# Kernel optimization log

Hardware: AMD Instinct MI355X
Metric: run time of the kernel (lower is better)

Reference implementation:

```python
import jax, jax.numpy as jnp
import numpy as np

ENC, STR_H, CELL_H, ATTN = 512, 256, 512, 512
B, L = 64, 1024


def setup_inputs() -> dict:
    key = jax.random.key(0)
    ks = jax.random.split(key, 12)
    s = lambda fan_in: 1.0 / np.sqrt(fan_in)
    return {
        "encoded_features_map": jax.random.normal(ks[0], (B, L, ENC), jnp.float32),
        "structural_hidden_state": jax.random.normal(ks[1], (1, B, STR_H), jnp.float32),
        "cell_content_hidden_state": jax.random.normal(ks[2], (1, B, CELL_H), jnp.float32),
        "W_enc": jax.random.uniform(ks[3], (ENC, ATTN), jnp.float32, -s(ENC), s(ENC)),
        "b_enc": jax.random.uniform(ks[4], (ATTN,), jnp.float32, -s(ENC), s(ENC)),
        "W_str": jax.random.uniform(ks[5], (STR_H, ATTN), jnp.float32, -s(STR_H), s(STR_H)),
        "b_str": jax.random.uniform(ks[6], (ATTN,), jnp.float32, -s(STR_H), s(STR_H)),
        "W_cell": jax.random.uniform(ks[7], (CELL_H, ATTN), jnp.float32, -s(CELL_H), s(CELL_H)),
        "b_cell": jax.random.uniform(ks[8], (ATTN,), jnp.float32, -s(CELL_H), s(CELL_H)),
        "W_comb": jax.random.uniform(ks[9], (ATTN, 1), jnp.float32, -s(ATTN), s(ATTN)),
        "b_comb": jax.random.uniform(ks[10], (1,), jnp.float32, -s(ATTN), s(ATTN)),
    }


def reference(encoded_features_map, structural_hidden_state, cell_content_hidden_state,
              W_enc, b_enc, W_str, b_str, W_cell, b_cell, W_comb, b_comb):
    # [B, L, A] projection of encoder features
    a_enc = jnp.einsum("ble,ea->bla", encoded_features_map, W_enc) + b_enc
    # [B, A] projections of the two hidden states (squeeze layer dim)
    a_str = structural_hidden_state[0] @ W_str + b_str
    a_cell = cell_content_hidden_state[0] @ W_cell + b_cell
    # broadcast add + ReLU + scalar score: [B, L]
    h = jax.nn.relu(a_enc + a_str[:, None, :] + a_cell[:, None, :])
    scores = jnp.einsum("bla,ao->bl", h, W_comb) + b_comb[0]
    weights = jax.nn.softmax(scores, axis=1)  # over sequence dim
    # weighted sum over L -> [B, ENC]
    context = jnp.einsum("bl,ble->be", weights, encoded_features_map)
    return context
```

## Files before the change

### kernel.cpp

```cpp
#include <hip/hip_runtime.h>
#include <stdint.h>

#define ENC_D 512
#define ATTN_D 512
#define STR_D 256
#define CELL_D 512
#define BATCH 64
#define SEQ 1024
#define NROWS (BATCH * SEQ)

typedef __bf16 bf16x8 __attribute__((ext_vector_type(8)));
typedef float f32x4 __attribute__((ext_vector_type(4)));

__device__ __forceinline__ unsigned short f2bf(float f) {
    unsigned int u = __float_as_uint(f);
    u += 0x7fffu + ((u >> 16) & 1u);
    return (unsigned short)(u >> 16);
}

__device__ __forceinline__ bf16x8 cvt8(const float4 a, const float4 b) {
    bf16x8 r;
    r[0] = (__bf16)a.x; r[1] = (__bf16)a.y; r[2] = (__bf16)a.z; r[3] = (__bf16)a.w;
    r[4] = (__bf16)b.x; r[5] = (__bf16)b.y; r[6] = (__bf16)b.z; r[7] = (__bf16)b.w;
    return r;
}

__device__ __forceinline__ void lds_cp16(void* l, const void* g) {
    __builtin_amdgcn_global_load_lds(
        (const __attribute__((address_space(1))) unsigned int*)g,
        (__attribute__((address_space(3))) unsigned int*)l, 16, 0, 0);
}

#define BAR_VM4() asm volatile("s_waitcnt vmcnt(4)\n\ts_barrier" ::: "memory")
#define BAR_VM0() asm volatile("s_waitcnt vmcnt(0)\n\ts_barrier" ::: "memory")

__global__ __launch_bounds__(256) void k_prep(const float* __restrict__ W,
                                              unsigned short* __restrict__ WF,
                                              const float* __restrict__ str,
                                              const float* __restrict__ cell,
                                              const float* __restrict__ Wstr,
                                              const float* __restrict__ Wcell,
                                              float* __restrict__ bpart) {
    __shared__ char smraw[64 * 68 * 2];
    const int bx = blockIdx.x, t = threadIdx.x;

    if (bx < 64) {
        unsigned short* T = (unsigned short*)smraw;
        const int ei = bx >> 3, ni = bx & 7;
        const int e0 = ei * 64, n0 = ni * 64;
#pragma unroll
        for (int i = 0; i < 4; ++i) {
            const int idx = t + i * 256;
            const int r = idx >> 4, c4 = idx & 15;
            const float4 v = *(const float4*)(W + (size_t)(e0 + r) * ATTN_D + n0 + c4 * 4);
            T[(c4 * 4 + 0) * 68 + r] = f2bf(v.x);
            T[(c4 * 4 + 1) * 68 + r] = f2bf(v.y);
            T[(c4 * 4 + 2) * 68 + r] = f2bf(v.z);
            T[(c4 * 4 + 3) * 68 + r] = f2bf(v.w);
        }
        __syncthreads();
#pragma unroll
        for (int i = 0; i < 2; ++i) {
            const int q = t + i * 256;
            const int n = q >> 3, ge = q & 7;
            union { unsigned short s[8]; uint4 u; } o;
#pragma unroll
            for (int j = 0; j < 8; ++j) o.s[j] = T[n * 68 + ge * 8 + j];
            const int ng = n0 + n;
            const int g = ei * 8 + ge;
            const int nt = ng >> 4, c = ng & 15;
            const int ks = g >> 2, quad = g & 3;
            const int gi = nt * 1024 + ks * 64 + quad * 16 + c;
            *(uint4*)(WF + (size_t)gi * 8) = o.u;
        }
    } else {
        float* sj = (float*)smraw;
        float* red = (float*)smraw + 64;
        const int q = bx - 64;
        const int b = q / 12, jq = q - b * 12;
        const float* hvec;
        const float* Wbase;
        if (jq < 4) { hvec = str + b * STR_D + jq * 64;         Wbase = Wstr + (size_t)(jq * 64) * ATTN_D; }
        else        { hvec = cell + b * CELL_D + (jq - 4) * 64; Wbase = Wcell + (size_t)((jq - 4) * 64) * ATTN_D; }
        if (t < 64) sj[t] = hvec[t];
        __syncthreads();
        const int h = t >> 7, a4 = t & 127;
        f32x4 acc = {0.f, 0.f, 0.f, 0.f};
#pragma unroll 8
        for (int i = h * 32; i < h * 32 + 32; ++i) {
            const float s = sj[i];
            const float4 wv = *(const float4*)(Wbase + (size_t)i * ATTN_D + a4 * 4);
            acc[0] += s * wv.x; acc[1] += s * wv.y; acc[2] += s * wv.z; acc[3] += s * wv.w;
        }
        if (h == 1) *(f32x4*)(red + a4 * 4) = acc;
        __syncthreads();
        if (h == 0) {
            const f32x4 o = *(const f32x4*)(red + a4 * 4);
            acc[0] += o[0]; acc[1] += o[1]; acc[2] += o[2]; acc[3] += o[3];
            *(f32x4*)(bpart + (size_t)(jq * BATCH + b) * ATTN_D + a4 * 4) = acc;
        }
    }
}

__global__ __launch_bounds__(512, 1) void k_scores(const float* __restrict__ E,
                                                   const unsigned short* __restrict__ WF,
                                                   const float* __restrict__ bpart,
                                                   const float* __restrict__ b_enc,
                                                   const float* __restrict__ b_str,
                                                   const float* __restrict__ b_cell,
                                                   const float* __restrict__ Wcomb,
                                                   float* __restrict__ ctxp,
                                                   float* __restrict__ stats) {
    __shared__ unsigned short buf[3][16384];
    __shared__ float sbias[512];
    __shared__ float sWc[512];
    __shared__ float sx[256];
    __shared__ float ex[256];
    __shared__ float red[3][512];
    __shared__ float rtmp[8];

    const int tid = threadIdx.x;
    const int r0 = blockIdx.x * 256;
    const int b = blockIdx.x >> 2;
    const int w = tid >> 6, lane = tid & 63;
    const int quad = lane >> 4, c = lane & 15;

#pragma unroll
    for (int p = 0; p < 2; ++p)
#pragma unroll
        for (int i = 0; i < 4; ++i)
            lds_cp16((char*)&buf[p][0] + i * 8192 + tid * 16,
                     (const char*)WF + (size_t)p * 32768 + i * 8192 + tid * 16);

    if (tid < 128) {
        const int a = tid * 4;
        const float4 be = *(const float4*)(b_enc + a);
        const float4 bs = *(const float4*)(b_str + a);
        const float4 bc = *(const float4*)(b_cell + a);
        f32x4 s;
        s[0] = be.x + bs.x + bc.x; s[1] = be.y + bs.y + bc.y;
        s[2] = be.z + bs.z + bc.z; s[3] = be.w + bs.w + bc.w;
#pragma unroll
        for (int jq = 0; jq < 12; ++jq) {
            const float4 p = *(const float4*)(bpart + (size_t)(jq * BATCH + b) * ATTN_D + a);
            s[0] += p.x; s[1] += p.y; s[2] += p.z; s[3] += p.w;
        }
        *(f32x4*)(sbias + a) = s;
        const float4 wcv = *(const float4*)(Wcomb + a);
        f32x4 wc4; wc4[0] = wcv.x; wc4[1] = wcv.y; wc4[2] = wcv.z; wc4[3] = wcv.w;
        *(f32x4*)(sWc + a) = wc4;
    }

    bf16x8 afr[2][16];
#pragma unroll
    for (int m = 0; m < 2; ++m) {
        const float* Ep = E + (size_t)(r0 + w * 32 + m * 16 + c) * ENC_D + quad * 8;
#pragma unroll
        for (int ks = 0; ks < 16; ++ks) {
            const float4 v0 = *(const float4*)(Ep + ks * 32);
            const float4 v1 = *(const float4*)(Ep + ks * 32 + 4);
            afr[m][ks] = cvt8(v0, v1);
        }
    }

    float sc0[4] = {0.f, 0.f, 0.f, 0.f};
    float sc1[4] = {0.f, 0.f, 0.f, 0.f};

    __syncthreads();

    int cbuf = 0, sbuf = 2;
    for (int ch = 0; ch < 16; ++ch) {
        if (ch < 14) {
            const char* gsrc = (const char*)WF + (size_t)(ch + 2) * 32768;
            char* ldst = (char*)&buf[sbuf][0];
#pragma unroll
            for (int i = 0; i < 4; ++i)
                lds_cp16(ldst + i * 8192 + tid * 16, gsrc + i * 8192 + tid * 16);
        }

        const unsigned short* wb = &buf[cbuf][0];
        f32x4 a0e = {0.f,0.f,0.f,0.f}, a0o = {0.f,0.f,0.f,0.f};
        f32x4 a1e = {0.f,0.f,0.f,0.f}, a1o = {0.f,0.f,0.f,0.f};
        f32x4 b0e = {0.f,0.f,0.f,0.f}, b0o = {0.f,0.f,0.f,0.f};
        f32x4 b1e = {0.f,0.f,0.f,0.f}, b1o = {0.f,0.f,0.f,0.f};
#pragma unroll
        for (int ks = 0; ks < 16; ks += 4) {
            const bf16x8 f0 = *(const bf16x8*)(wb + ((ks + 0) * 64 + lane) * 8);
            const bf16x8 f1 = *(const bf16x8*)(wb + ((ks + 1) * 64 + lane) * 8);
            const bf16x8 f2 = *(const bf16x8*)(wb + ((ks + 2) * 64 + lane) * 8);
            const bf16x8 f3 = *(const bf16x8*)(wb + ((ks + 3) * 64 + lane) * 8);
            const bf16x8 g0 = *(const bf16x8*)(wb + 8192 + ((ks + 0) * 64 + lane) * 8);
            const bf16x8 g1 = *(const bf16x8*)(wb + 8192 + ((ks + 1) * 64 + lane) * 8);
            const bf16x8 g2 = *(const bf16x8*)(wb + 8192 + ((ks + 2) * 64 + lane) * 8);
            const bf16x8 g3 = *(const bf16x8*)(wb + 8192 + ((ks + 3) * 64 + lane) * 8);
            a0e = __builtin_amdgcn_mfma_f32_16x16x32_bf16(afr[0][ks + 0], f0, a0e, 0, 0, 0);
            a1e = __builtin_amdgcn_mfma_f32_16x16x32_bf16(afr[1][ks + 0], f0, a1e, 0, 0, 0);
            a0o = __builtin_amdgcn_mfma_f32_16x16x32_bf16(afr[0][ks + 1], f1, a0o, 0, 0, 0);
            a1o = __builtin_amdgcn_mfma_f32_16x16x32_bf16(afr[1][ks + 1], f1, a1o, 0, 0, 0);
            b0e = __builtin_amdgcn_mfma_f32_16x16x32_bf16(afr[0][ks + 0], g0, b0e, 0, 0, 0);
            b1e = __builtin_amdgcn_mfma_f32_16x16x32_bf16(afr[1][ks + 0], g0, b1e, 0, 0, 0);
            b0o = __builtin_amdgcn_mfma_f32_16x16x32_bf16(afr[0][ks + 1], g1, b0o, 0, 0, 0);
            b1o = __builtin_amdgcn_mfma_f32_16x16x32_bf16(afr[1][ks + 1], g1, b1o, 0, 0, 0);
            a0e = __builtin_amdgcn_mfma_f32_16x16x32_bf16(afr[0][ks + 2], f2, a0e, 0, 0, 0);
            a1e = __builtin_amdgcn_mfma_f32_16x16x32_bf16(afr[1][ks + 2], f2, a1e, 0, 0, 0);
            a0o = __builtin_amdgcn_mfma_f32_16x16x32_bf16(afr[0][ks + 3], f3, a0o, 0, 0, 0);
            a1o = __builtin_amdgcn_mfma_f32_16x16x32_bf16(afr[1][ks + 3], f3, a1o, 0, 0, 0);
            b0e = __builtin_amdgcn_mfma_f32_16x16x32_bf16(afr[0][ks + 2], g2, b0e, 0, 0, 0);
            b1e = __builtin_amdgcn_mfma_f32_16x16x32_bf16(afr[1][ks + 2], g2, b1e, 0, 0, 0);
            b0o = __builtin_amdgcn_mfma_f32_16x16x32_bf16(afr[0][ks + 3], g3, b0o, 0, 0, 0);
            b1o = __builtin_amdgcn_mfma_f32_16x16x32_bf16(afr[1][ks + 3], g3, b1o, 0, 0, 0);
        }

        const int n0 = ch * 32 + c;
        const float bi0 = sbias[n0], wc0 = sWc[n0];
        const float bi1 = sbias[n0 + 16], wc1 = sWc[n0 + 16];
#pragma unroll
        for (int r = 0; r < 4; ++r) {
            float v;
            v = (a0e[r] + a0o[r]) + bi0; sc0[r] += (v > 0.f ? v : 0.f) * wc0;
            v = (b0e[r] + b0o[r]) + bi1; sc0[r] += (v > 0.f ? v : 0.f) * wc1;
            v = (a1e[r] + a1o[r]) + bi0; sc1[r] += (v > 0.f ? v : 0.f) * wc0;
            v = (b1e[r] + b1o[r]) + bi1; sc1[r] += (v > 0.f ? v : 0.f) * wc1;
        }

        cbuf = (cbuf == 2) ? 0 : cbuf + 1;
        sbuf = (sbuf == 2) ? 0 : sbuf + 1;
        if (ch < 15) {
            if (ch < 14) BAR_VM4();
            else         BAR_VM0();
        }
    }

#pragma unroll
    for (int r = 0; r < 4; ++r) {
        float v0 = sc0[r], v1 = sc1[r];
        v0 += __shfl_xor(v0, 1); v1 += __shfl_xor(v1, 1);
        v0 += __shfl_xor(v0, 2); v1 += __shfl_xor(v1, 2);
        v0 += __shfl_xor(v0, 4); v1 += __shfl_xor(v1, 4);
        sc0[r] = v0 + __shfl_xor(v0, 8);
        sc1[r] = v1 + __shfl_xor(v1, 8);
    }
    if (c == 0) {
        const int l0 = w * 32 + quad * 4;
#pragma unroll
        for (int r = 0; r < 4; ++r) sx[l0 + r] = sc0[r];
#pragma unroll
        for (int r = 0; r < 4; ++r) sx[l0 + 16 + r] = sc1[r];
    }
    __syncthreads();

    if (tid < 256) {
        float v = sx[tid];
        float mm = v;
#pragma unroll
        for (int o = 32; o > 0; o >>= 1) mm = fmaxf(mm, __shfl_xor(mm, o));
        if (lane == 0) rtmp[w] = mm;
    }
    __syncthreads();
    const float m_p = fmaxf(fmaxf(rtmp[0], rtmp[1]), fmaxf(rtmp[2], rtmp[3]));
    if (tid < 256) {
        const float e = __expf(sx[tid] - m_p);
        ex[tid] = e;
        float ss = e;
#pragma unroll
        for (int o = 32; o > 0; o >>= 1) ss += __shfl_xor(ss, o);
        if (lane == 0) rtmp[4 + w] = ss;
    }
    __syncthreads();
    if (tid == 0) {
        stats[blockIdx.x * 2 + 0] = m_p;
        stats[blockIdx.x * 2 + 1] = rtmp[4] + rtmp[5] + rtmp[6] + rtmp[7];
    }

    {
        const int g = tid >> 7, col4 = tid & 127;
        const float* Ep = E + (size_t)(r0 + g * 64) * ENC_D + col4 * 4;
        f32x4 accA = {0.f, 0.f, 0.f, 0.f};
        f32x4 accB = {0.f, 0.f, 0.f, 0.f};
#pragma unroll 8
        for (int l = 0; l < 64; l += 2) {
            const float4 eA = *(const float4*)(Ep + (size_t)l * ENC_D);
            const float4 eB = *(const float4*)(Ep + (size_t)(l + 1) * ENC_D);
            const float wA = ex[g * 64 + l];
            const float wB = ex[g * 64 + l + 1];
            accA[0] += wA * eA.x; accA[1] += wA * eA.y;
            accA[2] += wA * eA.z; accA[3] += wA * eA.w;
            accB[0] += wB * eB.x; accB[1] += wB * eB.y;
            accB[2] += wB * eB.z; accB[3] += wB * eB.w;
        }
        f32x4 acc;
        acc[0] = accA[0] + accB[0]; acc[1] = accA[1] + accB[1];
        acc[2] = accA[2] + accB[2]; acc[3] = accA[3] + accB[3];
        if (g > 0) *(f32x4*)(&red[g - 1][col4 * 4]) = acc;
        __syncthreads();
        if (g == 0) {
            const f32x4 r1 = *(const f32x4*)(&red[0][col4 * 4]);
            const f32x4 r2 = *(const f32x4*)(&red[1][col4 * 4]);
            const f32x4 r3 = *(const f32x4*)(&red[2][col4 * 4]);
            acc[0] += r1[0] + r2[0] + r3[0];
            acc[1] += r1[1] + r2[1] + r3[1];
            acc[2] += r1[2] + r2[2] + r3[2];
            acc[3] += r1[3] + r2[3] + r3[3];
            *(f32x4*)(ctxp + (size_t)blockIdx.x * 512 + col4 * 4) = acc;
        }
    }
}

__global__ __launch_bounds__(128) void k_final(const float* __restrict__ ctxp,
                                               const float* __restrict__ stats,
                                               float* __restrict__ out) {
    const int b = blockIdx.x, t = threadIdx.x;
    const float m0 = stats[(b * 4 + 0) * 2], z0 = stats[(b * 4 + 0) * 2 + 1];
    const float m1 = stats[(b * 4 + 1) * 2], z1 = stats[(b * 4 + 1) * 2 + 1];
    const float m2 = stats[(b * 4 + 2) * 2], z2 = stats[(b * 4 + 2) * 2 + 1];
    const float m3 = stats[(b * 4 + 3) * 2], z3 = stats[(b * 4 + 3) * 2 + 1];
    const float m = fmaxf(fmaxf(m0, m1), fmaxf(m2, m3));
    const float a0 = __expf(m0 - m), a1 = __expf(m1 - m);
    const float a2 = __expf(m2 - m), a3 = __expf(m3 - m);
    const float invD = 1.f / (z0 * a0 + z1 * a1 + z2 * a2 + z3 * a3);

    const float4 c0 = *(const float4*)(ctxp + (size_t)(b * 4 + 0) * 512 + t * 4);
    const float4 c1 = *(const float4*)(ctxp + (size_t)(b * 4 + 1) * 512 + t * 4);
    const float4 c2 = *(const float4*)(ctxp + (size_t)(b * 4 + 2) * 512 + t * 4);
    const float4 c3 = *(const float4*)(ctxp + (size_t)(b * 4 + 3) * 512 + t * 4);
    f32x4 o;
    o[0] = (c0.x * a0 + c1.x * a1 + c2.x * a2 + c3.x * a3) * invD;
    o[1] = (c0.y * a0 + c1.y * a1 + c2.y * a2 + c3.y * a3) * invD;
    o[2] = (c0.z * a0 + c1.z * a1 + c2.z * a2 + c3.z * a3) * invD;
    o[3] = (c0.w * a0 + c1.w * a1 + c2.w * a2 + c3.w * a3) * invD;
    *(f32x4*)(out + (size_t)b * ENC_D + t * 4) = o;
}

extern "C" void kernel_launch(void* const* d_in, const int* in_sizes, int n_in,
                              void* d_out, int out_size, void* d_ws, size_t ws_size,
                              hipStream_t stream) {
    const float* E      = (const float*)d_in[0];
    const float* str    = (const float*)d_in[1];
    const float* cell   = (const float*)d_in[2];
    const float* Wenc   = (const float*)d_in[3];
    const float* b_enc  = (const float*)d_in[4];
    const float* Wstr   = (const float*)d_in[5];
    const float* b_str  = (const float*)d_in[6];
    const float* Wcell  = (const float*)d_in[7];
    const float* b_cell = (const float*)d_in[8];
    const float* Wcomb  = (const float*)d_in[9];
    float* out = (float*)d_out;

    char* ws = (char*)d_ws;
    unsigned short* WF = (unsigned short*)ws;
    float* bpart = (float*)(ws + (512 << 10));
    float* ctxp  = (float*)(ws + (512 << 10) + (1536 << 10));
    float* stats = (float*)(ws + (512 << 10) + (2048 << 10));

    k_prep<<<832, 256, 0, stream>>>(Wenc, WF, str, cell, Wstr, Wcell, bpart);
    k_scores<<<NROWS / 256, 512, 0, stream>>>(E, WF, bpart, b_enc, b_str, b_cell, Wcomb, ctxp, stats);
    k_final<<<BATCH, 128, 0, stream>>>(ctxp, stats, out);
}
```

Baseline: 262.8 us.

## Stage encoder A-fragments through LDS with pipelined async global-to-LDS copies

The A operand (encoder rows) was loaded with direct per-lane float4 global loads and converted to bf16 in registers. It is now streamed into a per-wave LDS staging area with async global_load_lds copies, double-buffered in 8 pieces with vmcnt waits, then read back from LDS and converted. The shared memory is merged into one raw region so this staging can reuse the space later taken by the weight triple buffer. The aim is more outstanding memory traffic and better-coalesced global reads. The cost is extra LDS round trips, an added barrier, and a larger shared footprint.

Measured after the change: 270.0 us. 1.03x slower.

```diff
diff --git a/kernel.cpp b/kernel.cpp
--- a/kernel.cpp
+++ b/kernel.cpp
@@ -33,6 +33,8 @@
 
 #define BAR_VM4() asm volatile("s_waitcnt vmcnt(4)\n\ts_barrier" ::: "memory")
 #define BAR_VM0() asm volatile("s_waitcnt vmcnt(0)\n\ts_barrier" ::: "memory")
+#define WAIT_VM8() asm volatile("s_waitcnt vmcnt(8)" ::: "memory")
+#define WAIT_VM0() asm volatile("s_waitcnt vmcnt(0)" ::: "memory")
 
 __global__ __launch_bounds__(256) void k_prep(const float* __restrict__ W,
                                               unsigned short* __restrict__ WF,
@@ -111,25 +113,68 @@
                                                    const float* __restrict__ Wcomb,
                                                    float* __restrict__ ctxp,
                                                    float* __restrict__ stats) {
-    __shared__ unsigned short buf[3][16384];
-    __shared__ float sbias[512];
-    __shared__ float sWc[512];
-    __shared__ float sx[256];
-    __shared__ float ex[256];
-    __shared__ float red[3][512];
-    __shared__ float rtmp[8];
+    __shared__ char smem[131072 + 12352];
+    float* sbias = (float*)(smem + 131072);
+    float* sWc   = (float*)(smem + 131072 + 2048);
+    float* sx    = (float*)(smem + 131072 + 4096);
+    float* ex    = (float*)(smem + 131072 + 5120);
+    float* redp  = (float*)(smem + 131072 + 6144);
+    float* rtmp  = (float*)(smem + 131072 + 12288);
 
     const int tid = threadIdx.x;
     const int r0 = blockIdx.x * 256;
     const int b = blockIdx.x >> 2;
     const int w = tid >> 6, lane = tid & 63;
     const int quad = lane >> 4, c = lane & 15;
+    const int rl0 = lane & 15;
+    const int cqv = lane >> 4;
+
+    bf16x8 afr[2][16];
+    {
+        char* Ab = smem + w * 16384;
+        const float* Esrc = E + (size_t)(r0 + w * 32) * ENC_D;
+
+#define ISSUE_PIECE(sp)                                                        \
+        do {                                                                   \
+            char* dst_ = Ab + (((sp) & 1) ? 8192 : 0);                         \
+            _Pragma("unroll")                                                  \
+            for (int i = 0; i < 8; ++i) {                                      \
+                const int row_ = rl0 + ((i & 1) << 4);                         \
+                const int colq_ = (sp) * 16 + cqv + ((i >> 1) << 2);           \
+                lds_cp16(dst_ + i * 1024 + lane * 16,                          \
+                         Esrc + (size_t)row_ * ENC_D + colq_ * 4);             \
+            }                                                                  \
+        } while (0)
+
+        ISSUE_PIECE(0);
+        ISSUE_PIECE(1);
+#pragma unroll
+        for (int s = 0; s < 8; ++s) {
+            if (s < 7) WAIT_VM8();
+            else       WAIT_VM0();
+            const char* Pb = Ab + ((s & 1) ? 8192 : 0);
+#pragma unroll
+            for (int m = 0; m < 2; ++m)
+#pragma unroll
+                for (int d = 0; d < 2; ++d) {
+                    const int x0 = d * 8 + quad * 2;
+                    const int x1 = x0 + 1;
+                    const float4 g0 = *(const float4*)(Pb + (m + 2 * (x0 >> 2)) * 1024 + (c + 16 * (x0 & 3)) * 16);
+                    const float4 g1 = *(const float4*)(Pb + (m + 2 * (x1 >> 2)) * 1024 + (c + 16 * (x1 & 3)) * 16);
+                    afr[m][2 * s + d] = cvt8(g0, g1);
+                }
+            if (s < 6) ISSUE_PIECE(s + 2);
+        }
+#undef ISSUE_PIECE
+    }
+
+    __syncthreads();
 
 #pragma unroll
     for (int p = 0; p < 2; ++p)
 #pragma unroll
         for (int i = 0; i < 4; ++i)
-            lds_cp16((char*)&buf[p][0] + i * 8192 + tid * 16,
+            lds_cp16(smem + p * 32768 + i * 8192 + tid * 16,
                      (const char*)WF + (size_t)p * 32768 + i * 8192 + tid * 16);
 
     if (tid < 128) {
@@ -151,18 +196,6 @@
         *(f32x4*)(sWc + a) = wc4;
     }
 
-    bf16x8 afr[2][16];
-#pragma unroll
-    for (int m = 0; m < 2; ++m) {
-        const float* Ep = E + (size_t)(r0 + w * 32 + m * 16 + c) * ENC_D + quad * 8;
-#pragma unroll
-        for (int ks = 0; ks < 16; ++ks) {
-            const float4 v0 = *(const float4*)(Ep + ks * 32);
-            const float4 v1 = *(const float4*)(Ep + ks * 32 + 4);
-            afr[m][ks] = cvt8(v0, v1);
-        }
-    }
-
     float sc0[4] = {0.f, 0.f, 0.f, 0.f};
     float sc1[4] = {0.f, 0.f, 0.f, 0.f};
 
@@ -172,13 +205,13 @@
     for (int ch = 0; ch < 16; ++ch) {
         if (ch < 14) {
             const char* gsrc = (const char*)WF + (size_t)(ch + 2) * 32768;
-            char* ldst = (char*)&buf[sbuf][0];
+            char* ldst = smem + sbuf * 32768;
 #pragma unroll
             for (int i = 0; i < 4; ++i)
                 lds_cp16(ldst + i * 8192 + tid * 16, gsrc + i * 8192 + tid * 16);
         }
 
-        const unsigned short* wb = &buf[cbuf][0];
+        const unsigned short* wb = (const unsigned short*)(smem + cbuf * 32768);
         f32x4 a0e = {0.f,0.f,0.f,0.f}, a0o = {0.f,0.f,0.f,0.f};
         f32x4 a1e = {0.f,0.f,0.f,0.f}, a1o = {0.f,0.f,0.f,0.f};
         f32x4 b0e = {0.f,0.f,0.f,0.f}, b0o = {0.f,0.f,0.f,0.f};
@@ -189,10 +222,10 @@
             const bf16x8 f1 = *(const bf16x8*)(wb + ((ks + 1) * 64 + lane) * 8);
             const bf16x8 f2 = *(const bf16x8*)(wb + ((ks + 2) * 64 + lane) * 8);
             const bf16x8 f3 = *(const bf16x8*)(wb + ((ks + 3) * 64 + lane) * 8);
-            const bf16x8 g0 = *(const bf16x8*)(wb + 8192 + ((ks + 0) * 64 + lane) * 8);
-            const bf16x8 g1 = *(const bf16x8*)(wb + 8192 + ((ks + 1) * 64 + lane) * 8);
-            const bf16x8 g2 = *(const bf16x8*)(wb + 8192 + ((ks + 2) * 64 + lane) * 8);
-            const bf16x8 g3 = *(const bf16x8*)(wb + 8192 + ((ks + 3) * 64 + lane) * 8);
+            const bf16x8 g0 = *(const bf16x8*)(wb + 4096 * 2 + ((ks + 0) * 64 + lane) * 8);
+            const bf16x8 g1 = *(const bf16x8*)(wb + 4096 * 2 + ((ks + 1) * 64 + lane) * 8);
+            const bf16x8 g2 = *(const bf16x8*)(wb + 4096 * 2 + ((ks + 2) * 64 + lane) * 8);
+            const bf16x8 g3 = *(const bf16x8*)(wb + 4096 * 2 + ((ks + 3) * 64 + lane) * 8);
             a0e = __builtin_amdgcn_mfma_f32_16x16x32_bf16(afr[0][ks + 0], f0, a0e, 0, 0, 0);
             a1e = __builtin_amdgcn_mfma_f32_16x16x32_bf16(afr[1][ks + 0], f0, a1e, 0, 0, 0);
             a0o = __builtin_amdgcn_mfma_f32_16x16x32_bf16(afr[0][ks + 1], f1, a0o, 0, 0, 0);
@@ -291,12 +324,12 @@
         f32x4 acc;
         acc[0] = accA[0] + accB[0]; acc[1] = accA[1] + accB[1];
         acc[2] = accA[2] + accB[2]; acc[3] = accA[3] + accB[3];
-        if (g > 0) *(f32x4*)(&red[g - 1][col4 * 4]) = acc;
+        if (g > 0) *(f32x4*)(redp + (g - 1) * 512 + col4 * 4) = acc;
         __syncthreads();
         if (g == 0) {
-            const f32x4 r1 = *(const f32x4*)(&red[0][col4 * 4]);
-            const f32x4 r2 = *(const f32x4*)(&red[1][col4 * 4]);
-            const f32x4 r3 = *(const f32x4*)(&red[2][col4 * 4]);
+            const f32x4 r1 = *(const f32x4*)(redp + 0 * 512 + col4 * 4);
+            const f32x4 r2 = *(const f32x4*)(redp + 1 * 512 + col4 * 4);
+            const f32x4 r3 = *(const f32x4*)(redp + 2 * 512 + col4 * 4);
             acc[0] += r1[0] + r2[0] + r3[0];
             acc[1] += r1[1] + r2[1] + r3[1];
             acc[2] += r1[2] + r2[2] + r3[2];
```

## Fuse final softmax-merge into scores kernel via last-block atomic counter

Applied to the files above, without the earlier changes.

Removes the separate k_final launch. Each scores block increments a per-batch atomic counter, and the last of the four blocks for a batch merges the partial max/sum stats and context into the output. The counter is reset by an extra block in k_prep. The diff also batches all the encoder-feature loads before the bf16 conversions, split by a sched_barrier, so more memory requests are in flight at once. This adds threadfence and atomic cost per block and a serial tail in the last block.

Result: slower. 323.7 us (+23.2%).

```diff
diff --git a/kernel.cpp b/kernel.cpp
--- a/kernel.cpp
+++ b/kernel.cpp
@@ -40,7 +40,8 @@
                                               const float* __restrict__ cell,
                                               const float* __restrict__ Wstr,
                                               const float* __restrict__ Wcell,
-                                              float* __restrict__ bpart) {
+                                              float* __restrict__ bpart,
+                                              unsigned int* __restrict__ cnt) {
     __shared__ char smraw[64 * 68 * 2];
     const int bx = blockIdx.x, t = threadIdx.x;
 
@@ -73,7 +74,7 @@
             const int gi = nt * 1024 + ks * 64 + quad * 16 + c;
             *(uint4*)(WF + (size_t)gi * 8) = o.u;
         }
-    } else {
+    } else if (bx < 832) {
         float* sj = (float*)smraw;
         float* red = (float*)smraw + 64;
         const int q = bx - 64;
@@ -99,6 +100,8 @@
             acc[0] += o[0]; acc[1] += o[1]; acc[2] += o[2]; acc[3] += o[3];
             *(f32x4*)(bpart + (size_t)(jq * BATCH + b) * ATTN_D + a4 * 4) = acc;
         }
+    } else {
+        if (t < BATCH) cnt[t] = 0u;
     }
 }
 
@@ -110,7 +113,9 @@
                                                    const float* __restrict__ b_cell,
                                                    const float* __restrict__ Wcomb,
                                                    float* __restrict__ ctxp,
-                                                   float* __restrict__ stats) {
+                                                   float* __restrict__ stats,
+                                                   unsigned int* __restrict__ cnt,
+                                                   float* __restrict__ out) {
     __shared__ unsigned short buf[3][16384];
     __shared__ float sbias[512];
     __shared__ float sWc[512];
@@ -118,6 +123,7 @@
     __shared__ float ex[256];
     __shared__ float red[3][512];
     __shared__ float rtmp[8];
+    __shared__ int lastf;
 
     const int tid = threadIdx.x;
     const int r0 = blockIdx.x * 256;
@@ -155,12 +161,16 @@
 #pragma unroll
     for (int m = 0; m < 2; ++m) {
         const float* Ep = E + (size_t)(r0 + w * 32 + m * 16 + c) * ENC_D + quad * 8;
+        float4 t0[16], t1[16];
 #pragma unroll
         for (int ks = 0; ks < 16; ++ks) {
-            const float4 v0 = *(const float4*)(Ep + ks * 32);
-            const float4 v1 = *(const float4*)(Ep + ks * 32 + 4);
-            afr[m][ks] = cvt8(v0, v1);
-        }
+            t0[ks] = *(const float4*)(Ep + ks * 32);
+            t1[ks] = *(const float4*)(Ep + ks * 32 + 4);
+        }
+        __builtin_amdgcn_sched_barrier(0);
+#pragma unroll
+        for (int ks = 0; ks < 16; ++ks)
+            afr[m][ks] = cvt8(t0[ks], t1[ks]);
     }
 
     float sc0[4] = {0.f, 0.f, 0.f, 0.f};
@@ -304,31 +314,30 @@
             *(f32x4*)(ctxp + (size_t)blockIdx.x * 512 + col4 * 4) = acc;
         }
     }
-}
-
-__global__ __launch_bounds__(128) void k_final(const float* __restrict__ ctxp,
-                                               const float* __restrict__ stats,
-                                               float* __restrict__ out) {
-    const int b = blockIdx.x, t = threadIdx.x;
-    const float m0 = stats[(b * 4 + 0) * 2], z0 = stats[(b * 4 + 0) * 2 + 1];
-    const float m1 = stats[(b * 4 + 1) * 2], z1 = stats[(b * 4 + 1) * 2 + 1];
-    const float m2 = stats[(b * 4 + 2) * 2], z2 = stats[(b * 4 + 2) * 2 + 1];
-    const float m3 = stats[(b * 4 + 3) * 2], z3 = stats[(b * 4 + 3) * 2 + 1];
-    const float m = fmaxf(fmaxf(m0, m1), fmaxf(m2, m3));
-    const float a0 = __expf(m0 - m), a1 = __expf(m1 - m);
-    const float a2 = __expf(m2 - m), a3 = __expf(m3 - m);
-    const float invD = 1.f / (z0 * a0 + z1 * a1 + z2 * a2 + z3 * a3);
-
-    const float4 c0 = *(const float4*)(ctxp + (size_t)(b * 4 + 0) * 512 + t * 4);
-    const float4 c1 = *(const float4*)(ctxp + (size_t)(b * 4 + 1) * 512 + t * 4);
-    const float4 c2 = *(const float4*)(ctxp + (size_t)(b * 4 + 2) * 512 + t * 4);
-    const float4 c3 = *(const float4*)(ctxp + (size_t)(b * 4 + 3) * 512 + t * 4);
-    f32x4 o;
-    o[0] = (c0.x * a0 + c1.x * a1 + c2.x * a2 + c3.x * a3) * invD;
-    o[1] = (c0.y * a0 + c1.y * a1 + c2.y * a2 + c3.y * a3) * invD;
-    o[2] = (c0.z * a0 + c1.z * a1 + c2.z * a2 + c3.z * a3) * invD;
-    o[3] = (c0.w * a0 + c1.w * a1 + c2.w * a2 + c3.w * a3) * invD;
-    *(f32x4*)(out + (size_t)b * ENC_D + t * 4) = o;
+
+    __threadfence();
+    __syncthreads();
+    if (tid == 0) lastf = (atomicAdd(&cnt[b], 1u) == 3u) ? 1 : 0;
+    __syncthreads();
+    if (lastf) {
+        __threadfence();
+        float mp[4], zp[4];
+#pragma unroll
+        for (int p = 0; p < 4; ++p) {
+            mp[p] = stats[(b * 4 + p) * 2];
+            zp[p] = stats[(b * 4 + p) * 2 + 1];
+        }
+        const float m = fmaxf(fmaxf(mp[0], mp[1]), fmaxf(mp[2], mp[3]));
+        float a[4], D = 0.f;
+#pragma unroll
+        for (int p = 0; p < 4; ++p) { a[p] = __expf(mp[p] - m); D += zp[p] * a[p]; }
+        const float invD = 1.f / D;
+        float o = 0.f;
+#pragma unroll
+        for (int p = 0; p < 4; ++p)
+            o += ctxp[(size_t)(b * 4 + p) * 512 + tid] * a[p];
+        out[(size_t)b * ENC_D + tid] = o * invD;
+    }
 }
 
 extern "C" void kernel_launch(void* const* d_in, const int* in_sizes, int n_in,
@@ -351,8 +360,9 @@
     float* bpart = (float*)(ws + (512 << 10));
     float* ctxp  = (float*)(ws + (512 << 10) + (1536 << 10));
     float* stats = (float*)(ws + (512 << 10) + (2048 << 10));
-
-    k_prep<<<832, 256, 0, stream>>>(Wenc, WF, str, cell, Wstr, Wcell, bpart);
-    k_scores<<<NROWS / 256, 512, 0, stream>>>(E, WF, bpart, b_enc, b_str, b_cell, Wcomb, ctxp, stats);
-    k_final<<<BATCH, 128, 0, stream>>>(ctxp, stats, out);
-}
+    unsigned int* cnt = (unsigned int*)(ws + (512 << 10) + (2048 << 10) + 4096);
+
+    k_prep<<<833, 256, 0, stream>>>(Wenc, WF, str, cell, Wstr, Wcell, bpart, cnt);
+    k_scores<<<NROWS / 256, 512, 0, stream>>>(E, WF, bpart, b_enc, b_str, b_cell,
+                                              Wcomb, ctxp, stats, cnt, out);
+}
```
